# Kernel tuning notes

Hardware: AMD Instinct MI355X
Metric: run time of the kernel (lower is better)

## Reference

```python
import jax, jax.numpy as jnp
import numpy as np

DIM = 1024
NUM_HEADS = 16
HEAD_DIM = DIM // NUM_HEADS
LN_EPS = 1e-5


def setup_inputs() -> dict:
    key = jax.random.key(0)
    ks = jax.random.split(key, 12)
    B, S = 2, 2048
    queries = jax.random.normal(ks[0], (B, S, DIM), dtype=jnp.float32)
    keys = jax.random.normal(ks[1], (B, S, DIM), dtype=jnp.float32)
    values = jax.random.normal(ks[2], (B, S, DIM), dtype=jnp.float32)
    # per-head Linear(dim, head_dim) weights stacked over heads: [H, dim, head_dim]
    scale = 1.0 / np.sqrt(DIM)
    Wq = jax.random.uniform(ks[3], (NUM_HEADS, DIM, HEAD_DIM), jnp.float32, -scale, scale)
    bq = jax.random.uniform(ks[4], (NUM_HEADS, HEAD_DIM), jnp.float32, -scale, scale)
    Wk = jax.random.uniform(ks[5], (NUM_HEADS, DIM, HEAD_DIM), jnp.float32, -scale, scale)
    bk = jax.random.uniform(ks[6], (NUM_HEADS, HEAD_DIM), jnp.float32, -scale, scale)
    Wv = jax.random.uniform(ks[7], (NUM_HEADS, DIM, HEAD_DIM), jnp.float32, -scale, scale)
    bv = jax.random.uniform(ks[8], (NUM_HEADS, HEAD_DIM), jnp.float32, -scale, scale)
    gamma = jnp.ones((DIM,), dtype=jnp.float32)
    beta = jnp.zeros((DIM,), dtype=jnp.float32)
    return {"queries": queries, "keys": keys, "values": values,
            "Wq": Wq, "bq": bq, "Wk": Wk, "bk": bk, "Wv": Wv, "bv": bv,
            "gamma": gamma, "beta": beta}


def reference(queries, keys, values, Wq, bq, Wk, bk, Wv, bv, gamma, beta):
    # Per-head projections fused as a single batched GEMM over heads.
    # q/k/v: [B, H, S, head_dim]  (dropout is identity in eval mode)
    q = jnp.einsum('bsd,hdk->bhsk', queries, Wq) + bq[None, :, None, :]
    k = jnp.einsum('bsd,hdk->bhsk', keys, Wk) + bk[None, :, None, :]
    v = jnp.einsum('bsd,hdk->bhsk', values, Wv) + bv[None, :, None, :]
    # scores: [B, H, S, S], scaled by 1/sqrt(head_dim)
    scores = jnp.einsum('bhsk,bhtk->bhst', q, k) / jnp.sqrt(jnp.float32(HEAD_DIM))
    probs = jax.nn.softmax(scores, axis=-1)
    attended = jnp.einsum('bhst,bhtk->bhsk', probs, v)  # [B, H, S, head_dim]
    # concat heads -> [B, S, dim]
    B, H, S, K = attended.shape
    attended = attended.transpose(0, 2, 1, 3).reshape(B, S, H * K)
    # LayerNorm over last dim
    mean = jnp.mean(attended, axis=-1, keepdims=True)
    var = jnp.mean(jnp.square(attended - mean), axis=-1, keepdims=True)
    normed = (attended - mean) * jax.lax.rsqrt(var + LN_EPS)
    return normed * gamma + beta
```

## Files before the change

kernel.cpp:

```cpp
#include <hip/hip_runtime.h>

#define B_ 2
#define S_ 2048
#define D_ 1024
#define H_ 16
#define HD_ 64

typedef unsigned short u16;
typedef short bf16x8 __attribute__((ext_vector_type(8)));
typedef float f32x4 __attribute__((ext_vector_type(4)));

union FragU { bf16x8 v; u16 u[8]; uint2 d2[2]; unsigned w[4]; uint4 q; };

__device__ __forceinline__ u16 f2bf(float f) {
  unsigned int x = __builtin_bit_cast(unsigned int, f);
  x += 0x7fffu + ((x >> 16) & 1u);
  return (u16)(x >> 16);
}

__device__ __forceinline__ float fexp2(float x) {
  return __builtin_amdgcn_exp2f(x);
}

__device__ __forceinline__ void g2l(const void* g, void* l) {
  __builtin_amdgcn_global_load_lds(
      (const __attribute__((address_space(1))) unsigned int*)g,
      (__attribute__((address_space(3))) unsigned int*)l, 16, 0, 0);
}

#define MFMA16(a, b, c) __builtin_amdgcn_mfma_f32_16x16x32_bf16(a, b, c, 0, 0, 0)

#define KPERM(m) ((((m) & 15) >> 2) * 8 + (((m) >> 4) << 2) + ((m) & 3))

__global__ __launch_bounds__(256) void prep_kernel(
    const float* __restrict__ Wq, const float* __restrict__ Wk,
    const float* __restrict__ Wv, u16* __restrict__ WT)
{
  const int blk = blockIdx.x;
  const int z = blk >> 6, h = (blk >> 2) & 15, qtr = blk & 3;
  const float* src = ((z == 0) ? Wq : (z == 1) ? Wk : Wv) + (size_t)h * D_ * HD_;
  u16* dst = WT + (size_t)z * D_ * D_ + (size_t)h * HD_ * D_;
  const int tid = threadIdx.x;
  const int n = tid & 63, kh = tid >> 6;
  #pragma unroll
  for (int k32 = qtr * 2; k32 < qtr * 2 + 2; ++k32) {
    const int kbase = kh * 256 + k32 * 32;
    union { u16 u[32]; uint4 q[4]; } pk;
    #pragma unroll
    for (int m = 0; m < 32; ++m)
      pk.u[KPERM(m)] = f2bf(src[(size_t)(kbase + m) * HD_ + n]);
    #pragma unroll
    for (int j = 0; j < 4; ++j)
      *(uint4*)(dst + (size_t)n * D_ + kbase + j * 8) = pk.q[j];
  }
}

__global__ __launch_bounds__(256) void proj_kernel(
    const float* __restrict__ Xq, const float* __restrict__ Xk, const float* __restrict__ Xv,
    const u16* __restrict__ WT,
    const float* __restrict__ bq, const float* __restrict__ bk, const float* __restrict__ bv,
    u16* __restrict__ qo, u16* __restrict__ ko, u16* __restrict__ vo)
{
  const int z = blockIdx.z;
  const int rowb = blockIdx.x;
  const int col  = blockIdx.y;
  const float* X  = (z == 0) ? Xq : (z == 1) ? Xk : Xv;
  const float* Bb = (z == 0) ? bq : (z == 1) ? bk : bv;
  u16* out = (z == 0) ? qo : (z == 1) ? ko : vo;
  const float scale = (z == 0) ? 0.125f * 1.44269504f : 1.0f;

  const int tid = threadIdx.x;
  const int l = tid & 63, w = tid >> 6;
  const int g = l >> 4, lr = l & 15;
  const int wm = w >> 1, wn = w & 1;

  __shared__ u16 As_[2][64 * 64];
  __shared__ u16 Bs_[2][128 * 64];

  const char* Wb = (const char*)(WT + (size_t)z * D_ * D_ + (size_t)col * 128 * D_);

  int bOff[4], bLds[4];
  #pragma unroll
  for (int i = 0; i < 4; ++i) {
    const int br = w * 32 + i * 8 + (l >> 3);
    bOff[i] = br * 2048 + (((l & 7) * 16) ^ ((br & 7) << 4));
    bLds[i] = (w * 4 + i) * 1024;
  }

  const int arow  = tid >> 2;
  const int aksub = (tid >> 1) & 1;
  const int ag0   = (tid & 1) * 2;
  const float* aSrc = X + (size_t)(rowb * 64 + arow) * D_ + aksub * 32 + ag0 * 4;
  const int asw = (arow & 7) << 4;
  const int aw0 = arow * 128 + ((aksub * 64 + ag0 * 16) ^ asw);
  const int aw1 = arow * 128 + ((aksub * 64 + (ag0 + 1) * 16) ^ asw);

  float4 a0, a1, a2, a3;

#define ALOAD(k0)                                                              \
  {                                                                            \
    const float* s = aSrc + (k0);                                              \
    a0 = *(const float4*)s;        a1 = *(const float4*)(s + 16);              \
    a2 = *(const float4*)(s + 4);  a3 = *(const float4*)(s + 20);              \
  }

#define AWRITE(buf)                                                            \
  {                                                                            \
    FragU t0, t1;                                                              \
    asm("v_cvt_pk_bf16_f32 %0, %1, %2" : "=v"(t0.w[0]) : "v"(a0.x), "v"(a0.y));\
    asm("v_cvt_pk_bf16_f32 %0, %1, %2" : "=v"(t0.w[1]) : "v"(a0.z), "v"(a0.w));\
    asm("v_cvt_pk_bf16_f32 %0, %1, %2" : "=v"(t0.w[2]) : "v"(a1.x), "v"(a1.y));\
    asm("v_cvt_pk_bf16_f32 %0, %1, %2" : "=v"(t0.w[3]) : "v"(a1.z), "v"(a1.w));\
    asm("v_cvt_pk_bf16_f32 %0, %1, %2" : "=v"(t1.w[0]) : "v"(a2.x), "v"(a2.y));\
    asm("v_cvt_pk_bf16_f32 %0, %1, %2" : "=v"(t1.w[1]) : "v"(a2.z), "v"(a2.w));\
    asm("v_cvt_pk_bf16_f32 %0, %1, %2" : "=v"(t1.w[2]) : "v"(a3.x), "v"(a3.y));\
    asm("v_cvt_pk_bf16_f32 %0, %1, %2" : "=v"(t1.w[3]) : "v"(a3.z), "v"(a3.w));\
    *(uint4*)((char*)As_[buf] + aw0) = t0.q;                                   \
    *(uint4*)((char*)As_[buf] + aw1) = t1.q;                                   \
  }

  ALOAD(0);
  AWRITE(0);
  #pragma unroll
  for (int i = 0; i < 4; ++i) g2l(Wb + bOff[i], (char*)Bs_[0] + bLds[i]);
  __syncthreads();

  const f32x4 zero = {0.f, 0.f, 0.f, 0.f};
  f32x4 acc[2][4];
  #pragma unroll
  for (int mt = 0; mt < 2; ++mt)
    #pragma unroll
    for (int nt = 0; nt < 4; ++nt) acc[mt][nt] = zero;

  for (int ks = 0; ks < 16; ++ks) {
    const int cur = ks & 1;
    if (ks < 15) {
      ALOAD((ks + 1) * 64);
      #pragma unroll
      for (int i = 0; i < 4; ++i)
        g2l(Wb + bOff[i] + (ks + 1) * 128, (char*)Bs_[cur ^ 1] + bLds[i]);
    }

    const char* Ac = (const char*)As_[cur];
    const char* Bc = (const char*)Bs_[cur];
    #pragma unroll
    for (int ksub = 0; ksub < 2; ++ksub) {
      FragU aF[2], bF[4];
      #pragma unroll
      for (int mt = 0; mt < 2; ++mt) {
        const int row = wm * 32 + mt * 16 + lr;
        aF[mt].v = *(const bf16x8*)(Ac + row * 128 +
                    ((ksub * 64 + g * 16) ^ ((row & 7) << 4)));
      }
      #pragma unroll
      for (int nt = 0; nt < 4; ++nt) {
        const int row = wn * 64 + nt * 16 + lr;
        bF[nt].v = *(const bf16x8*)(Bc + row * 128 +
                    ((ksub * 64 + g * 16) ^ ((row & 7) << 4)));
      }
      __builtin_amdgcn_s_setprio(1);
      #pragma unroll
      for (int mt = 0; mt < 2; ++mt)
        #pragma unroll
        for (int nt = 0; nt < 4; ++nt)
          acc[mt][nt] = MFMA16(aF[mt].v, bF[nt].v, acc[mt][nt]);
      __builtin_amdgcn_s_setprio(0);
    }

    if (ks < 15) AWRITE(cur ^ 1);
    __syncthreads();
  }

  #pragma unroll
  for (int nt = 0; nt < 4; ++nt) {
    const int ng = col * 128 + wn * 64 + nt * 16 + lr;
    const float bias = Bb[ng];
    const int h = ng >> 6, n = ng & 63;
    const int dperm = (n & 32) + ((n & 15) >> 2) * 8 + ((n & 16) >> 4) * 4 + (n & 3);
    #pragma unroll
    for (int mt = 0; mt < 2; ++mt) {
      const int R = rowb * 64 + wm * 32 + mt * 16 + g * 4;
      const int b = R >> 11, s0 = R & (S_ - 1);
      if (z < 2) {
        #pragma unroll
        for (int r = 0; r < 4; ++r)
          out[(((size_t)b * H_ + h) * S_ + s0 + r) * HD_ + dperm] =
              f2bf((acc[mt][nt][r] + bias) * scale);
      } else {
        const int a = (s0 >> 2) & 7;
        const int s0p = (s0 & ~31) + ((2 * (a & 3) + (a >> 2)) << 2);
        union { u16 u[4]; uint2 d; } pk;
        #pragma unroll
        for (int r = 0; r < 4; ++r) pk.u[r] = f2bf(acc[mt][nt][r] + bias);
        *(uint2*)(out + (((size_t)b * H_ + h) * HD_ + n) * S_ + s0p) = pk.d;
      }
    }
  }
#undef ALOAD
#undef AWRITE
}

__global__ __launch_bounds__(256) void attn_kernel(
    const u16* __restrict__ q, const u16* __restrict__ k,
    const u16* __restrict__ vt, u16* __restrict__ attP, float* __restrict__ lrow)
{
  const int bid = blockIdx.x;
  const int xcd = bid & 7;
  const int t1 = bid >> 3;
  const int qt = t1 & 15;
  const int bh = ((t1 >> 4) << 3) | xcd;

  const int tid = threadIdx.x;
  const int l = tid & 63, w = tid >> 6;
  const int g = l >> 4, lr = l & 15;
  const int qbase = qt * 128 + w * 32;

  #define BUFSZ (64 * 144)
  __shared__ __align__(16) char Ksm[2 * BUFSZ];
  __shared__ __align__(16) char Vsm[2 * BUFSZ];

  FragU qf[2][2];
  #pragma unroll
  for (int qg = 0; qg < 2; ++qg) {
    const char* qrow = (const char*)(q + ((size_t)bh * S_ + qbase + qg * 16 + lr) * HD_);
    qf[qg][0].v = *(const bf16x8*)(qrow + g * 16);
    qf[qg][1].v = *(const bf16x8*)(qrow + 64 + g * 16);
  }

  const char* kByte = (const char*)(k + (size_t)bh * S_ * HD_);
  const char* vByte = (const char*)(vt + (size_t)bh * HD_ * S_);

  const int i0 = tid * 16, i1 = i0 + 4096;
  const int r0 = i0 >> 7, c0 = i0 & 127;
  const int r1 = i1 >> 7, c1 = i1 & 127;
  char* kD0 = Ksm + r0 * 144 + c0;
  char* kD1 = Ksm + r1 * 144 + c1;
  char* vD0 = Vsm + r0 * 144 + c0;
  char* vD1 = Vsm + r1 * 144 + c1;
  const char* kS0 = kByte + i0;
  const char* kS1 = kByte + i1;
  const char* vS0 = vByte + (size_t)r0 * (S_ * 2) + c0;
  const char* vS1 = vByte + (size_t)r1 * (S_ * 2) + c1;

  uint4 kA = *(const uint4*)kS0;
  uint4 kB = *(const uint4*)kS1;
  uint4 vA = *(const uint4*)vS0;
  uint4 vB = *(const uint4*)vS1;
  *(uint4*)kD0 = kA; *(uint4*)kD1 = kB;
  *(uint4*)vD0 = vA; *(uint4*)vD1 = vB;
  __syncthreads();

  const f32x4 zero = {0.f, 0.f, 0.f, 0.f};
  f32x4 accO[2][4] = {{zero, zero, zero, zero}, {zero, zero, zero, zero}};
  float m_[2] = {-3e38f, -3e38f};
  float l_[2] = {0.f, 0.f};

  const char* kfb = Ksm + lr * 144 + g * 16;
  const char* vfb = Vsm + lr * 144 + g * 16;

  for (int t0 = 0; t0 < S_; t0 += 64) {
    const int cur = (t0 >> 6) & 1;
    const bool hasNext = (t0 + 64) < S_;
    if (hasNext) {
      kA = *(const uint4*)(kS0 + (t0 + 64) * 128);
      kB = *(const uint4*)(kS1 + (t0 + 64) * 128);
      vA = *(const uint4*)(vS0 + (t0 + 64) * 2);
      vB = *(const uint4*)(vS1 + (t0 + 64) * 2);
    }
    const char* kfbc = kfb + cur * BUFSZ;
    const char* vfbc = vfb + cur * BUFSZ;

    f32x4 sc[2][4] = {{zero, zero, zero, zero}, {zero, zero, zero, zero}};
    __builtin_amdgcn_s_setprio(1);
    #pragma unroll
    for (int ct = 0; ct < 4; ++ct) {
      FragU kf0, kf1;
      kf0.v = *(const bf16x8*)(kfbc + ct * 2304);
      kf1.v = *(const bf16x8*)(kfbc + ct * 2304 + 64);
      sc[0][ct] = MFMA16(kf0.v, qf[0][0].v, sc[0][ct]);
      sc[0][ct] = MFMA16(kf1.v, qf[0][1].v, sc[0][ct]);
      sc[1][ct] = MFMA16(kf0.v, qf[1][0].v, sc[1][ct]);
      sc[1][ct] = MFMA16(kf1.v, qf[1][1].v, sc[1][ct]);
    }
    __builtin_amdgcn_s_setprio(0);

    float lmax[2];
    #pragma unroll
    for (int qg = 0; qg < 2; ++qg) {
      float a0 = fmaxf(fmaxf(sc[qg][0][0], sc[qg][0][1]), fmaxf(sc[qg][0][2], sc[qg][0][3]));
      float a1 = fmaxf(fmaxf(sc[qg][1][0], sc[qg][1][1]), fmaxf(sc[qg][1][2], sc[qg][1][3]));
      float a2 = fmaxf(fmaxf(sc[qg][2][0], sc[qg][2][1]), fmaxf(sc[qg][2][2], sc[qg][2][3]));
      float a3 = fmaxf(fmaxf(sc[qg][3][0], sc[qg][3][1]), fmaxf(sc[qg][3][2], sc[qg][3][3]));
      lmax[qg] = fmaxf(fmaxf(a0, a1), fmaxf(a2, a3));
    }
    if (__any((lmax[0] - m_[0] > 8.f) || (lmax[1] - m_[1] > 8.f))) {
      #pragma unroll
      for (int qg = 0; qg < 2; ++qg) {
        float mm = lmax[qg];
        mm = fmaxf(mm, __shfl_xor(mm, 16));
        mm = fmaxf(mm, __shfl_xor(mm, 32));
        const float mn = fmaxf(m_[qg], mm);
        const float al = fexp2(m_[qg] - mn);
        m_[qg] = mn;
        l_[qg] *= al;
        float alr[4];
        #pragma unroll
        for (int r = 0; r < 4; ++r) alr[r] = __shfl(al, g * 4 + r);
        #pragma unroll
        for (int dt = 0; dt < 4; ++dt)
          #pragma unroll
          for (int r = 0; r < 4; ++r) accO[qg][dt][r] *= alr[r];
      }
    }

    FragU pf[2][2];
    #pragma unroll
    for (int qg = 0; qg < 2; ++qg) {
      #pragma unroll
      for (int ct = 0; ct < 4; ++ct)
        #pragma unroll
        for (int r = 0; r < 4; ++r)
          sc[qg][ct][r] = fexp2(sc[qg][ct][r] - m_[qg]);
      float s0 = (sc[qg][0][0] + sc[qg][0][1]) + (sc[qg][0][2] + sc[qg][0][3]);
      float s1 = (sc[qg][1][0] + sc[qg][1][1]) + (sc[qg][1][2] + sc[qg][1][3]);
      float s2 = (sc[qg][2][0] + sc[qg][2][1]) + (sc[qg][2][2] + sc[qg][2][3]);
      float s3 = (sc[qg][3][0] + sc[qg][3][1]) + (sc[qg][3][2] + sc[qg][3][3]);
      l_[qg] += (s0 + s1) + (s2 + s3);
      #pragma unroll
      for (int tc = 0; tc < 2; ++tc) {
        asm("v_cvt_pk_bf16_f32 %0, %1, %2" : "=v"(pf[qg][tc].w[0]) : "v"(sc[qg][2*tc][0]),   "v"(sc[qg][2*tc][1]));
        asm("v_cvt_pk_bf16_f32 %0, %1, %2" : "=v"(pf[qg][tc].w[1]) : "v"(sc[qg][2*tc][2]),   "v"(sc[qg][2*tc][3]));
        asm("v_cvt_pk_bf16_f32 %0, %1, %2" : "=v"(pf[qg][tc].w[2]) : "v"(sc[qg][2*tc+1][0]), "v"(sc[qg][2*tc+1][1]));
        asm("v_cvt_pk_bf16_f32 %0, %1, %2" : "=v"(pf[qg][tc].w[3]) : "v"(sc[qg][2*tc+1][2]), "v"(sc[qg][2*tc+1][3]));
      }
    }

    __builtin_amdgcn_s_setprio(1);
    #pragma unroll
    for (int dt = 0; dt < 4; ++dt) {
      FragU vf0, vf1;
      vf0.v = *(const bf16x8*)(vfbc + dt * 2304);
      vf1.v = *(const bf16x8*)(vfbc + dt * 2304 + 64);
      accO[0][dt] = MFMA16(pf[0][0].v, vf0.v, accO[0][dt]);
      accO[0][dt] = MFMA16(pf[0][1].v, vf1.v, accO[0][dt]);
      accO[1][dt] = MFMA16(pf[1][0].v, vf0.v, accO[1][dt]);
      accO[1][dt] = MFMA16(pf[1][1].v, vf1.v, accO[1][dt]);
    }
    __builtin_amdgcn_s_setprio(0);

    if (hasNext) {
      const int nb = (cur ^ 1) * BUFSZ;
      *(uint4*)(kD0 + nb) = kA; *(uint4*)(kD1 + nb) = kB;
      *(uint4*)(vD0 + nb) = vA; *(uint4*)(vD1 + nb) = vB;
    }
    __syncthreads();
  }

  const int b = bh >> 4, h = bh & (H_ - 1);
  u16* basep = attP + (size_t)b * S_ * D_;
  #pragma unroll
  for (int qg = 0; qg < 2; ++qg) {
    float lt = l_[qg];
    lt += __shfl_xor(lt, 16);
    lt += __shfl_xor(lt, 32);
    #pragma unroll
    for (int r = 0; r < 4; ++r) {
      const int s = qbase + qg * 16 + g * 4 + r;
      u16* op = basep + (size_t)s * D_ + h * HD_;
      #pragma unroll
      for (int dt = 0; dt < 4; ++dt) op[dt * 16 + lr] = f2bf(accO[qg][dt][r]);
    }
    if (g == 0)
      lrow[((size_t)b * H_ + h) * S_ + qbase + qg * 16 + lr] = lt;
  }
  #undef BUFSZ
}

__global__ __launch_bounds__(256) void combine_ln_kernel(
    const u16* __restrict__ attP, const float* __restrict__ lrow,
    const float* __restrict__ gamma, const float* __restrict__ beta,
    float* __restrict__ out)
{
  const int row = blockIdx.x;
  const int b = row >> 11, s = row & (S_ - 1);
  const int tid = threadIdx.x;
  const int h = tid >> 4;

  const float inv = 1.0f / lrow[((size_t)b * H_ + h) * S_ + s];
  union { uint2 d; u16 u[4]; } raw;
  raw.d = ((const uint2*)(attP + (size_t)row * D_))[tid];
  float4 x;
  x.x = __builtin_bit_cast(float, (unsigned)raw.u[0] << 16) * inv;
  x.y = __builtin_bit_cast(float, (unsigned)raw.u[1] << 16) * inv;
  x.z = __builtin_bit_cast(float, (unsigned)raw.u[2] << 16) * inv;
  x.w = __builtin_bit_cast(float, (unsigned)raw.u[3] << 16) * inv;

  float sm = x.x + x.y + x.z + x.w;
  float sq = x.x * x.x + x.y * x.y + x.z * x.z + x.w * x.w;
  #pragma unroll
  for (int j = 1; j < 64; j <<= 1) { sm += __shfl_xor(sm, j); sq += __shfl_xor(sq, j); }
  __shared__ float ls[4], lq[4];
  const int w = tid >> 6;
  if ((tid & 63) == 0) { ls[w] = sm; lq[w] = sq; }
  __syncthreads();
  if (tid == 0) {
    ls[0] = ls[0] + ls[1] + ls[2] + ls[3];
    lq[0] = lq[0] + lq[1] + lq[2] + lq[3];
  }
  __syncthreads();
  const float mean = ls[0] * (1.f / D_);
  const float var  = lq[0] * (1.f / D_) - mean * mean;
  const float rs = rsqrtf(var + 1e-5f);
  const float4 gv = ((const float4*)gamma)[tid];
  const float4 bv = ((const float4*)beta)[tid];
  float4 o;
  o.x = (x.x - mean) * rs * gv.x + bv.x;
  o.y = (x.y - mean) * rs * gv.y + bv.y;
  o.z = (x.z - mean) * rs * gv.z + bv.z;
  o.w = (x.w - mean) * rs * gv.w + bv.w;
  ((float4*)(out + (size_t)row * D_))[tid] = o;
}

extern "C" void kernel_launch(void* const* d_in, const int* in_sizes, int n_in,
                              void* d_out, int out_size, void* d_ws, size_t ws_size,
                              hipStream_t stream) {
  const float* queries = (const float*)d_in[0];
  const float* keys    = (const float*)d_in[1];
  const float* values  = (const float*)d_in[2];
  const float* Wq = (const float*)d_in[3];
  const float* bq = (const float*)d_in[4];
  const float* Wk = (const float*)d_in[5];
  const float* bk = (const float*)d_in[6];
  const float* Wv = (const float*)d_in[7];
  const float* bv = (const float*)d_in[8];
  const float* gamma = (const float*)d_in[9];
  const float* beta  = (const float*)d_in[10];
  float* out = (float*)d_out;

  const size_t PER = (size_t)B_ * H_ * S_ * HD_;
  u16* q_ws  = (u16*)d_ws;
  u16* k_ws  = q_ws + PER;
  u16* vt_ws = k_ws + PER;
  u16* WT   = vt_ws + PER;
  u16* attP = vt_ws + PER;
  const size_t NOUT = (size_t)B_ * S_ * D_;
  float* lrow = (float*)(attP + NOUT);

  prep_kernel<<<dim3(192), 256, 0, stream>>>(Wq, Wk, Wv, WT);
  proj_kernel<<<dim3(64, 8, 3), 256, 0, stream>>>(
      queries, keys, values, WT, bq, bk, bv, q_ws, k_ws, vt_ws);
  attn_kernel<<<dim3(512), 256, 0, stream>>>(q_ws, k_ws, vt_ws, attP, lrow);
  combine_ln_kernel<<<dim3(4096), 256, 0, stream>>>(attP, lrow, gamma, beta, out);
}
```

Measured before the change: 124.8 us.

## Split attention KV range across two blocks and merge partials in LayerNorm kernel

Adds a split-KV mode where each attention block processes half the key sequence, doubling the grid to 1024 blocks. Each split writes unnormalized partial outputs plus row max and sum, and the combine/LayerNorm kernel rescales and merges the two partials before normalization. This aims to raise parallelism and reduce tail imbalance on the attention kernel, at the cost of extra partial output traffic and workspace. It falls back to the single-split path if the workspace is too small.

Result: slower. 128.8 us (+3.3%).

```diff
diff --git a/kernel.cpp b/kernel.cpp
--- a/kernel.cpp
+++ b/kernel.cpp
@@ -200,15 +200,21 @@
 #undef AWRITE
 }
 
+template<int NSPLIT>
 __global__ __launch_bounds__(256) void attn_kernel(
     const u16* __restrict__ q, const u16* __restrict__ k,
-    const u16* __restrict__ vt, u16* __restrict__ attP, float* __restrict__ lrow)
+    const u16* __restrict__ vt, u16* __restrict__ attP, float2* __restrict__ ml)
 {
   const int bid = blockIdx.x;
   const int xcd = bid & 7;
   const int t1 = bid >> 3;
   const int qt = t1 & 15;
-  const int bh = ((t1 >> 4) << 3) | xcd;
+  const int u = t1 >> 4;
+  constexpr int SH = (NSPLIT == 2) ? 1 : 0;
+  const int split = u & (NSPLIT - 1);
+  const int bh = ((u >> SH) << 3) | xcd;
+  constexpr int TEND = S_ / NSPLIT;
+  const int tbase = split * TEND;
 
   const int tid = threadIdx.x;
   const int l = tid & 63, w = tid >> 6;
@@ -237,10 +243,10 @@
   char* kD1 = Ksm + r1 * 144 + c1;
   char* vD0 = Vsm + r0 * 144 + c0;
   char* vD1 = Vsm + r1 * 144 + c1;
-  const char* kS0 = kByte + i0;
-  const char* kS1 = kByte + i1;
-  const char* vS0 = vByte + (size_t)r0 * (S_ * 2) + c0;
-  const char* vS1 = vByte + (size_t)r1 * (S_ * 2) + c1;
+  const char* kS0 = kByte + (size_t)tbase * 128 + i0;
+  const char* kS1 = kByte + (size_t)tbase * 128 + i1;
+  const char* vS0 = vByte + (size_t)r0 * (S_ * 2) + tbase * 2 + c0;
+  const char* vS1 = vByte + (size_t)r1 * (S_ * 2) + tbase * 2 + c1;
 
   uint4 kA = *(const uint4*)kS0;
   uint4 kB = *(const uint4*)kS1;
@@ -258,9 +264,9 @@
   const char* kfb = Ksm + lr * 144 + g * 16;
   const char* vfb = Vsm + lr * 144 + g * 16;
 
-  for (int t0 = 0; t0 < S_; t0 += 64) {
+  for (int t0 = 0; t0 < TEND; t0 += 64) {
     const int cur = (t0 >> 6) & 1;
-    const bool hasNext = (t0 + 64) < S_;
+    const bool hasNext = (t0 + 64) < TEND;
     if (hasNext) {
       kA = *(const uint4*)(kS0 + (t0 + 64) * 128);
       kB = *(const uint4*)(kS1 + (t0 + 64) * 128);
@@ -357,7 +363,7 @@
   }
 
   const int b = bh >> 4, h = bh & (H_ - 1);
-  u16* basep = attP + (size_t)b * S_ * D_;
+  u16* basep = attP + (size_t)split * B_ * S_ * D_ + (size_t)b * S_ * D_;
   #pragma unroll
   for (int qg = 0; qg < 2; ++qg) {
     float lt = l_[qg];
@@ -370,14 +376,17 @@
       #pragma unroll
       for (int dt = 0; dt < 4; ++dt) op[dt * 16 + lr] = f2bf(accO[qg][dt][r]);
     }
-    if (g == 0)
-      lrow[((size_t)b * H_ + h) * S_ + qbase + qg * 16 + lr] = lt;
+    if (g == 0) {
+      float2 v; v.x = m_[qg]; v.y = lt;
+      ml[((size_t)split * B_ * H_ + (size_t)b * H_ + h) * S_ + qbase + qg * 16 + lr] = v;
+    }
   }
   #undef BUFSZ
 }
 
+template<int NSPLIT>
 __global__ __launch_bounds__(256) void combine_ln_kernel(
-    const u16* __restrict__ attP, const float* __restrict__ lrow,
+    const u16* __restrict__ attP, const float2* __restrict__ ml,
     const float* __restrict__ gamma, const float* __restrict__ beta,
     float* __restrict__ out)
 {
@@ -386,14 +395,32 @@
   const int tid = threadIdx.x;
   const int h = tid >> 4;
 
-  const float inv = 1.0f / lrow[((size_t)b * H_ + h) * S_ + s];
-  union { uint2 d; u16 u[4]; } raw;
-  raw.d = ((const uint2*)(attP + (size_t)row * D_))[tid];
   float4 x;
-  x.x = __builtin_bit_cast(float, (unsigned)raw.u[0] << 16) * inv;
-  x.y = __builtin_bit_cast(float, (unsigned)raw.u[1] << 16) * inv;
-  x.z = __builtin_bit_cast(float, (unsigned)raw.u[2] << 16) * inv;
-  x.w = __builtin_bit_cast(float, (unsigned)raw.u[3] << 16) * inv;
+  {
+    union { uint2 d; u16 u[4]; } r0u;
+    r0u.d = ((const uint2*)(attP + (size_t)row * D_))[tid];
+    const float2 a0 = ml[((size_t)b * H_ + h) * S_ + s];
+    float x0[4];
+    #pragma unroll
+    for (int j = 0; j < 4; ++j)
+      x0[j] = __builtin_bit_cast(float, (unsigned)r0u.u[j] << 16);
+    if (NSPLIT == 2) {
+      union { uint2 d; u16 u[4]; } r1u;
+      r1u.d = ((const uint2*)(attP + ((size_t)B_ * S_ + row) * D_))[tid];
+      const float2 a1 = ml[((size_t)B_ * H_ + (size_t)b * H_ + h) * S_ + s];
+      const float mmax = fmaxf(a0.x, a1.x);
+      const float al0 = fexp2(a0.x - mmax), al1 = fexp2(a1.x - mmax);
+      const float inv = 1.0f / (a0.y * al0 + a1.y * al1);
+      const float w0 = al0 * inv, w1 = al1 * inv;
+      x.x = x0[0] * w0 + __builtin_bit_cast(float, (unsigned)r1u.u[0] << 16) * w1;
+      x.y = x0[1] * w0 + __builtin_bit_cast(float, (unsigned)r1u.u[1] << 16) * w1;
+      x.z = x0[2] * w0 + __builtin_bit_cast(float, (unsigned)r1u.u[2] << 16) * w1;
+      x.w = x0[3] * w0 + __builtin_bit_cast(float, (unsigned)r1u.u[3] << 16) * w1;
+    } else {
+      const float inv = 1.0f / a0.y;
+      x.x = x0[0] * inv; x.y = x0[1] * inv; x.z = x0[2] * inv; x.w = x0[3] * inv;
+    }
+  }
 
   float sm = x.x + x.y + x.z + x.w;
   float sq = x.x * x.x + x.y * x.y + x.z * x.z + x.w * x.w;
@@ -444,11 +471,20 @@
   u16* WT   = vt_ws + PER;
   u16* attP = vt_ws + PER;
   const size_t NOUT = (size_t)B_ * S_ * D_;
-  float* lrow = (float*)(attP + NOUT);
+  const size_t NML  = (size_t)B_ * H_ * S_;
+  const size_t need2 = 3 * PER * 2 + 2 * NOUT * 2 + 2 * NML * 8;
 
   prep_kernel<<<dim3(192), 256, 0, stream>>>(Wq, Wk, Wv, WT);
   proj_kernel<<<dim3(64, 8, 3), 256, 0, stream>>>(
       queries, keys, values, WT, bq, bk, bv, q_ws, k_ws, vt_ws);
-  attn_kernel<<<dim3(512), 256, 0, stream>>>(q_ws, k_ws, vt_ws, attP, lrow);
-  combine_ln_kernel<<<dim3(4096), 256, 0, stream>>>(attP, lrow, gamma, beta, out);
-}
+
+  if (ws_size >= need2) {
+    float2* ml = (float2*)(attP + 2 * NOUT);
+    attn_kernel<2><<<dim3(1024), 256, 0, stream>>>(q_ws, k_ws, vt_ws, attP, ml);
+    combine_ln_kernel<2><<<dim3(4096), 256, 0, stream>>>(attP, ml, gamma, beta, out);
+  } else {
+    float2* ml = (float2*)(attP + NOUT);
+    attn_kernel<1><<<dim3(512), 256, 0, stream>>>(q_ws, k_ws, vt_ws, attP, ml);
+    combine_ln_kernel<1><<<dim3(4096), 256, 0, stream>>>(attP, ml, gamma, beta, out);
+  }
+}
```

## Double KV tile size to 128 keys per iteration in attention loop

Applied to the files above, without the earlier changes.

Raises the key/value tile processed per loop iteration from 64 to 128 keys. This halves the number of barriers, online-softmax max/rescale checks, and loop overheads, and gives longer runs of MFMA work per tile. V shared-memory rows are widened to 272 bytes to hold 128 keys. The cost is roughly double the LDS footprint (about 70KB) and more registers for scores and prefetch, which may lower occupancy.

Measured after the change: 159.3 us. +27.7%, slower.

```diff
diff --git a/kernel.cpp b/kernel.cpp
--- a/kernel.cpp
+++ b/kernel.cpp
@@ -215,9 +215,10 @@
   const int g = l >> 4, lr = l & 15;
   const int qbase = qt * 128 + w * 32;
 
-  #define BUFSZ (64 * 144)
-  __shared__ __align__(16) char Ksm[2 * BUFSZ];
-  __shared__ __align__(16) char Vsm[2 * BUFSZ];
+  #define KBUF 18432
+  #define VBUF 17408
+  __shared__ __align__(16) char Ksm[2 * KBUF];
+  __shared__ __align__(16) char Vsm[2 * VBUF];
 
   FragU qf[2][2];
   #pragma unroll
@@ -230,24 +231,30 @@
   const char* kByte = (const char*)(k + (size_t)bh * S_ * HD_);
   const char* vByte = (const char*)(vt + (size_t)bh * HD_ * S_);
 
-  const int i0 = tid * 16, i1 = i0 + 4096;
-  const int r0 = i0 >> 7, c0 = i0 & 127;
-  const int r1 = i1 >> 7, c1 = i1 & 127;
-  char* kD0 = Ksm + r0 * 144 + c0;
-  char* kD1 = Ksm + r1 * 144 + c1;
-  char* vD0 = Vsm + r0 * 144 + c0;
-  char* vD1 = Vsm + r1 * 144 + c1;
-  const char* kS0 = kByte + i0;
-  const char* kS1 = kByte + i1;
-  const char* vS0 = vByte + (size_t)r0 * (S_ * 2) + c0;
-  const char* vS1 = vByte + (size_t)r1 * (S_ * 2) + c1;
-
-  uint4 kA = *(const uint4*)kS0;
-  uint4 kB = *(const uint4*)kS1;
-  uint4 vA = *(const uint4*)vS0;
-  uint4 vB = *(const uint4*)vS1;
-  *(uint4*)kD0 = kA; *(uint4*)kD1 = kB;
-  *(uint4*)vD0 = vA; *(uint4*)vD1 = vB;
+  char* kDst[4]; char* vDst[4];
+  const char* kSrc[4]; const char* vSrc[4];
+  #pragma unroll
+  for (int j = 0; j < 4; ++j) {
+    const int off = tid * 16 + j * 4096;
+    const int kr = off >> 7, kc = off & 127;
+    kDst[j] = Ksm + kr * 144 + kc;
+    kSrc[j] = kByte + off;
+    const int vr = off >> 8, vc = off & 255;
+    vDst[j] = Vsm + vr * 272 + vc;
+    vSrc[j] = vByte + (size_t)vr * (S_ * 2) + vc;
+  }
+
+  uint4 kR[4], vR[4];
+  #pragma unroll
+  for (int j = 0; j < 4; ++j) {
+    kR[j] = *(const uint4*)kSrc[j];
+    vR[j] = *(const uint4*)vSrc[j];
+  }
+  #pragma unroll
+  for (int j = 0; j < 4; ++j) {
+    *(uint4*)kDst[j] = kR[j];
+    *(uint4*)vDst[j] = vR[j];
+  }
   __syncthreads();
 
   const f32x4 zero = {0.f, 0.f, 0.f, 0.f};
@@ -256,24 +263,29 @@
   float l_[2] = {0.f, 0.f};
 
   const char* kfb = Ksm + lr * 144 + g * 16;
-  const char* vfb = Vsm + lr * 144 + g * 16;
-
-  for (int t0 = 0; t0 < S_; t0 += 64) {
-    const int cur = (t0 >> 6) & 1;
-    const bool hasNext = (t0 + 64) < S_;
+  const char* vfb = Vsm + lr * 272 + g * 16;
+
+  for (int t0 = 0; t0 < S_; t0 += 128) {
+    const int cur = (t0 >> 7) & 1;
+    const bool hasNext = (t0 + 128) < S_;
     if (hasNext) {
-      kA = *(const uint4*)(kS0 + (t0 + 64) * 128);
-      kB = *(const uint4*)(kS1 + (t0 + 64) * 128);
-      vA = *(const uint4*)(vS0 + (t0 + 64) * 2);
-      vB = *(const uint4*)(vS1 + (t0 + 64) * 2);
-    }
-    const char* kfbc = kfb + cur * BUFSZ;
-    const char* vfbc = vfb + cur * BUFSZ;
-
-    f32x4 sc[2][4] = {{zero, zero, zero, zero}, {zero, zero, zero, zero}};
+      #pragma unroll
+      for (int j = 0; j < 4; ++j) {
+        kR[j] = *(const uint4*)(kSrc[j] + (t0 + 128) * 128);
+        vR[j] = *(const uint4*)(vSrc[j] + (t0 + 128) * 2);
+      }
+    }
+    const char* kfbc = kfb + cur * KBUF;
+    const char* vfbc = vfb + cur * VBUF;
+
+    f32x4 sc[2][8];
+    #pragma unroll
+    for (int qg = 0; qg < 2; ++qg)
+      #pragma unroll
+      for (int ct = 0; ct < 8; ++ct) sc[qg][ct] = zero;
     __builtin_amdgcn_s_setprio(1);
     #pragma unroll
-    for (int ct = 0; ct < 4; ++ct) {
+    for (int ct = 0; ct < 8; ++ct) {
       FragU kf0, kf1;
       kf0.v = *(const bf16x8*)(kfbc + ct * 2304);
       kf1.v = *(const bf16x8*)(kfbc + ct * 2304 + 64);
@@ -287,11 +299,14 @@
     float lmax[2];
     #pragma unroll
     for (int qg = 0; qg < 2; ++qg) {
-      float a0 = fmaxf(fmaxf(sc[qg][0][0], sc[qg][0][1]), fmaxf(sc[qg][0][2], sc[qg][0][3]));
-      float a1 = fmaxf(fmaxf(sc[qg][1][0], sc[qg][1][1]), fmaxf(sc[qg][1][2], sc[qg][1][3]));
-      float a2 = fmaxf(fmaxf(sc[qg][2][0], sc[qg][2][1]), fmaxf(sc[qg][2][2], sc[qg][2][3]));
-      float a3 = fmaxf(fmaxf(sc[qg][3][0], sc[qg][3][1]), fmaxf(sc[qg][3][2], sc[qg][3][3]));
-      lmax[qg] = fmaxf(fmaxf(a0, a1), fmaxf(a2, a3));
+      float a[8];
+      #pragma unroll
+      for (int ct = 0; ct < 8; ++ct)
+        a[ct] = fmaxf(fmaxf(sc[qg][ct][0], sc[qg][ct][1]),
+                      fmaxf(sc[qg][ct][2], sc[qg][ct][3]));
+      float m01 = fmaxf(a[0], a[1]), m23 = fmaxf(a[2], a[3]);
+      float m45 = fmaxf(a[4], a[5]), m67 = fmaxf(a[6], a[7]);
+      lmax[qg] = fmaxf(fmaxf(m01, m23), fmaxf(m45, m67));
     }
     if (__any((lmax[0] - m_[0] > 8.f) || (lmax[1] - m_[1] > 8.f))) {
       #pragma unroll
@@ -313,21 +328,21 @@
       }
     }
 
-    FragU pf[2][2];
+    FragU pf[2][4];
     #pragma unroll
     for (int qg = 0; qg < 2; ++qg) {
       #pragma unroll
-      for (int ct = 0; ct < 4; ++ct)
+      for (int ct = 0; ct < 8; ++ct)
         #pragma unroll
         for (int r = 0; r < 4; ++r)
           sc[qg][ct][r] = fexp2(sc[qg][ct][r] - m_[qg]);
-      float s0 = (sc[qg][0][0] + sc[qg][0][1]) + (sc[qg][0][2] + sc[qg][0][3]);
-      float s1 = (sc[qg][1][0] + sc[qg][1][1]) + (sc[qg][1][2] + sc[qg][1][3]);
-      float s2 = (sc[qg][2][0] + sc[qg][2][1]) + (sc[qg][2][2] + sc[qg][2][3]);
-      float s3 = (sc[qg][3][0] + sc[qg][3][1]) + (sc[qg][3][2] + sc[qg][3][3]);
-      l_[qg] += (s0 + s1) + (s2 + s3);
-      #pragma unroll
-      for (int tc = 0; tc < 2; ++tc) {
+      float ssum = 0.f;
+      #pragma unroll
+      for (int ct = 0; ct < 8; ++ct)
+        ssum += (sc[qg][ct][0] + sc[qg][ct][1]) + (sc[qg][ct][2] + sc[qg][ct][3]);
+      l_[qg] += ssum;
+      #pragma unroll
+      for (int tc = 0; tc < 4; ++tc) {
         asm("v_cvt_pk_bf16_f32 %0, %1, %2" : "=v"(pf[qg][tc].w[0]) : "v"(sc[qg][2*tc][0]),   "v"(sc[qg][2*tc][1]));
         asm("v_cvt_pk_bf16_f32 %0, %1, %2" : "=v"(pf[qg][tc].w[1]) : "v"(sc[qg][2*tc][2]),   "v"(sc[qg][2*tc][3]));
         asm("v_cvt_pk_bf16_f32 %0, %1, %2" : "=v"(pf[qg][tc].w[2]) : "v"(sc[qg][2*tc+1][0]), "v"(sc[qg][2*tc+1][1]));
@@ -338,20 +353,26 @@
     __builtin_amdgcn_s_setprio(1);
     #pragma unroll
     for (int dt = 0; dt < 4; ++dt) {
-      FragU vf0, vf1;
-      vf0.v = *(const bf16x8*)(vfbc + dt * 2304);
-      vf1.v = *(const bf16x8*)(vfbc + dt * 2304 + 64);
-      accO[0][dt] = MFMA16(pf[0][0].v, vf0.v, accO[0][dt]);
-      accO[0][dt] = MFMA16(pf[0][1].v, vf1.v, accO[0][dt]);
-      accO[1][dt] = MFMA16(pf[1][0].v, vf0.v, accO[1][dt]);
-      accO[1][dt] = MFMA16(pf[1][1].v, vf1.v, accO[1][dt]);
+      FragU vf[4];
+      #pragma unroll
+      for (int tc = 0; tc < 4; ++tc)
+        vf[tc].v = *(const bf16x8*)(vfbc + dt * 4352 + tc * 64);
+      #pragma unroll
+      for (int tc = 0; tc < 4; ++tc) {
+        accO[0][dt] = MFMA16(pf[0][tc].v, vf[tc].v, accO[0][dt]);
+        accO[1][dt] = MFMA16(pf[1][tc].v, vf[tc].v, accO[1][dt]);
+      }
     }
     __builtin_amdgcn_s_setprio(0);
 
     if (hasNext) {
-      const int nb = (cur ^ 1) * BUFSZ;
-      *(uint4*)(kD0 + nb) = kA; *(uint4*)(kD1 + nb) = kB;
-      *(uint4*)(vD0 + nb) = vA; *(uint4*)(vD1 + nb) = vB;
+      const int kb = ((cur ^ 1) ? KBUF : 0);
+      const int vb = ((cur ^ 1) ? VBUF : 0);
+      #pragma unroll
+      for (int j = 0; j < 4; ++j) {
+        *(uint4*)(kDst[j] + kb) = kR[j];
+        *(uint4*)(vDst[j] + vb) = vR[j];
+      }
     }
     __syncthreads();
   }
@@ -373,7 +394,8 @@
     if (g == 0)
       lrow[((size_t)b * H_ + h) * S_ + qbase + qg * 16 + lr] = lt;
   }
-  #undef BUFSZ
+  #undef KBUF
+  #undef VBUF
 }
 
 __global__ __launch_bounds__(256) void combine_ln_kernel(
```
